# Optimization experiments

Measured on AMD Instinct MI355X. Metric: run time of the kernel, lower is better.

Reference implementation:

```python
import jax, jax.numpy as jnp
import numpy as np


def _shift(x, k):
    # roll time axis forward by k, zero-filling the first k steps
    if k == 0:
        return x
    return jnp.pad(x, ((0, 0), (k, 0), (0, 0)))[:, : x.shape[1]]


def _stu_conv(u, v, n):
    # u: (B,L,D), v: (L,K) spectral filters; non-tensordot branch of conv()
    B, L, D = u.shape
    K = v.shape[1]
    sgn = jnp.where(jnp.arange(L) % 2 == 1, -1.0, 1.0).astype(jnp.float32)[None, :, None, None]
    ue = jnp.broadcast_to(u[:, :, None, :], (B, L, K, D)).astype(jnp.float32)
    U = jnp.stack([ue, ue * sgn], axis=-1)                     # (B,L,K,D,2)
    Uf = jnp.fft.rfft(U, n=n, axis=1)
    vf = jnp.fft.rfft(v.astype(jnp.float32)[None, :, :, None, None], n=n, axis=1)
    Uc = jnp.fft.irfft(vf * Uf, n=n, axis=1)[:, :L]            # (B,L,K,D,2)
    U_plus = Uc[..., 0]
    U_minus = Uc[..., 1] * sgn
    return U_plus.astype(u.dtype), U_minus.astype(u.dtype)


def setup_inputs() -> dict:
    key = jax.random.key(0)
    ks = jax.random.split(key, 6)
    B, L, D, K, k_u, k_y = 2, 1024, 512, 16, 3, 2
    u = jax.random.normal(ks[0], (B, L, D), jnp.float32)
    filters = jax.random.normal(ks[1], (L, K), jnp.float32) / np.float32(np.sqrt(L))
    M_u = jax.random.normal(ks[2], (D, k_u, D), jnp.float32) * 0.01
    M_y = jax.random.normal(ks[3], (D, k_y, D), jnp.float32) * 0.01
    M_phi_plus = jax.random.normal(ks[4], (K, D, D), jnp.float32) * 0.01
    M_phi_minus = jax.random.normal(ks[5], (K, D, D), jnp.float32) * 0.01
    return {"u": u, "filters": filters, "M_u": M_u, "M_y": M_y,
            "M_phi_plus": M_phi_plus, "M_phi_minus": M_phi_minus}


def reference(u, filters, M_u, M_y, M_phi_plus, M_phi_minus):
    B, L, D = u.shape
    n = 1 << int(np.ceil(np.log2(2 * L - 1)))  # nearest power of two >= 2L-1
    k_u = M_u.shape[1]
    k_y = M_y.shape[1]

    # FFT-based long convolution with the +/- sign trick
    U_plus, U_minus = _stu_conv(u, filters, n)
    spectral = (jnp.einsum('blkd,kdo->blo', U_plus, M_phi_plus)
                + jnp.einsum('blkd,kdo->blo', U_minus, M_phi_minus))

    # input-AR term of compute_ar_strict: sum_j u[t+1-j] @ M_u[:, j-1].T (shifts 0..k_u-1)
    u_sh = jnp.stack([_shift(u, j - 1) for j in range(1, k_u + 1)], axis=1)  # (B,k_u,L,D)
    y_in = jnp.einsum('bjlf,ijf->bli', u_sh, M_u)

    z = spectral + y_in  # (B,L,D)

    # output-AR recurrence of compute_ar_strict as a scan
    def step(y_buf, z_t):
        y_t = z_t + jnp.einsum('bjf,djf->bd', y_buf, M_y)
        y_buf = jnp.concatenate([y_t[:, None], y_buf[:, :-1]], axis=1)
        return y_buf, y_t

    _, ys = jax.lax.scan(step, jnp.zeros((B, k_y, D), z.dtype), jnp.swapaxes(z, 0, 1))
    return jnp.swapaxes(ys, 0, 1)  # (B,L,D)
```

## Files before the change

kernel.cpp:

```cpp
#include <hip/hip_runtime.h>
#include <hip/hip_bf16.h>


using bf16 = __hip_bfloat16;
typedef __attribute__((ext_vector_type(8))) short bf16x8;
typedef __attribute__((ext_vector_type(4))) float f32x4;

#define B_   2
#define L_   1024
#define D_   512
#define K_   16
#define KT   17920
#define ROWS 2048
#define NTAP 6
#define PBLD 3584
#define SPLITD 14
#define SPLITR 6
#define ZBROWS 1032
#define NKS 40
#define NTD 20
#define WZOFF 4194304

#define WAIT_VM6 0x0F76
#define WAIT_VM4 0x0F74
#define WAIT_VM0 0x0F70

__device__ __forceinline__ void gll16(const void* g, void* l) {
    __builtin_amdgcn_global_load_lds(
        (const __attribute__((address_space(1))) unsigned int*)g,
        (__attribute__((address_space(3))) unsigned int*)l, 16, 0, 0);
}

__global__ void prep_all(const float* __restrict__ u, const float* __restrict__ fil,
                         const float* __restrict__ Mu, const float* __restrict__ My,
                         const float* __restrict__ Mp, const float* __restrict__ Mm,
                         bf16* __restrict__ U, bf16* __restrict__ BT,
                         bf16* __restrict__ PB, bf16* __restrict__ W,
                         bf16* __restrict__ Myb, bf16* __restrict__ BTT,
                         bf16* __restrict__ uPT) {
    __shared__ bf16 t[64][72];
    int bid = blockIdx.x, tid = threadIdx.x;
    auto pack4 = [](float4 v) {
        ushort4 o; bf16 h;
        h = __float2bfloat16(v.x); o.x = *(unsigned short*)&h;
        h = __float2bfloat16(v.y); o.y = *(unsigned short*)&h;
        h = __float2bfloat16(v.z); o.z = *(unsigned short*)&h;
        h = __float2bfloat16(v.w); o.w = *(unsigned short*)&h;
        return o;
    };
    if (bid < 3072) {
        int e4 = bid * 256 + tid;
        int r = e4 / 384, rem = e4 % 384;
        int tt = rem >> 7, f = (rem & 127) * 4;
        int b = r >> 10, l = r & 1023;
        float4 v = {0.f, 0.f, 0.f, 0.f};
        if (l >= tt) v = *(const float4*)&u[((size_t)b * L_ + l - tt) * D_ + f];
        *(ushort4*)&U[(size_t)r * KT + 16384 + tt * 512 + f] = pack4(v);
    } else if (bid < 3840) {
        int e4 = (bid - 3072) * 256 + tid;
        int o = e4 / 384, tf4 = (e4 % 384) * 4;
        float4 v = *(const float4*)&Mu[(size_t)o * 1536 + tf4];
        *(ushort4*)&BT[(size_t)o * KT + 16384 + tf4] = pack4(v);
    } else if (bid < 4352) {
        int e4 = (bid - 3840) * 256 + tid;
        int n = e4 >> 8, c4 = (e4 & 255) * 4;
        float4 v;
        if (c4 < 512) {
            v.x = (n == c4) ? 1.f : 0.f;     v.y = (n == c4 + 1) ? 1.f : 0.f;
            v.z = (n == c4 + 2) ? 1.f : 0.f; v.w = (n == c4 + 3) ? 1.f : 0.f;
        } else v = *(const float4*)&My[(size_t)n * 1024 + (c4 - 512)];
        *(ushort4*)&PB[(size_t)n * PBLD + c4] = pack4(v);
    } else if (bid < 5120) {
        int tile = bid - 4352;
        int set = tile >> 8, rem = tile & 255;
        int k = rem >> 4, g = (rem >> 2) & 3, kb = rem & 3;
        for (int idx = tid; idx < 4096; idx += 256) {
            int i = idx >> 5, jp = idx & 31;
            int j = ((jp >> 3) ^ ((i >> 1) & 3)) * 8 + (jp & 7);
            int x = g * 128 + i - kb * 32 - j - (set == 2 ? 1 : 0);
            float v = 0.f;
            if (x >= 0) {
                int row = (set == 0) ? 2 * x : 2 * x + 1;
                v = fil[row * K_ + k];
            }
            W[(size_t)tile * 4096 + idx] = __float2bfloat16(v);
        }
    } else if (bid < 5632) {
        int e4 = (bid - 5120) * 256 + tid;
        float4 v = *(const float4*)&My[(size_t)e4 * 4];
        *(ushort4*)&Myb[(size_t)e4 * 4] = pack4(v);
    } else if (bid < 7872) {
        int tt = bid - 5632;
        int zb = tt >> 6, rem = tt & 63;
        int bx = rem & 7, by = rem >> 3;
        int col = tid & 63, r0 = (tid >> 6) * 16;
        if (zb < 32) {
            int dt = bx * 64, ot = by * 64, c = zb;
            int k = c & 15;
            const float* sp = Mp + (size_t)k * D_ * D_;
            const float* sm = Mm + (size_t)k * D_ * D_;
            float sg = (c < 16) ? 1.f : -1.f;
            for (int i = 0; i < 16; ++i) {
                size_t o_ = (size_t)(dt + r0 + i) * D_ + ot + col;
                t[r0 + i][col] = __float2bfloat16(sp[o_] + sg * sm[o_]);
            }
            __syncthreads();
            for (int i = 0; i < 16; ++i)
                BT[(size_t)(ot + r0 + i) * KT + c * D_ + dt + col] = t[col][r0 + i];
        } else if (zb < 34) {
            int h = zb - 32;
            int dt = bx * 64, ft = by * 64;
            for (int i = 0; i < 16; ++i)
                t[r0 + i][col] = __float2bfloat16(My[(size_t)(dt + r0 + i) * 1024 + (1 - h) * 512 + ft + col]);
            __syncthreads();
            for (int i = 0; i < 16; ++i)
                BTT[(size_t)(ft + r0 + i) * 1024 + h * 512 + dt + col] = t[col][r0 + i];
        } else {
            for (int it = 0; it < 4; ++it) {
                int b = it >> 1, p = it & 1;
                int mt = bx * 64, dt = by * 64;
                __syncthreads();
                for (int i = 0; i < 16; ++i)
                    t[r0 + i][col] = __float2bfloat16(u[((size_t)b * L_ + 2 * (mt + r0 + i) + p) * D_ + dt + col]);
                __syncthreads();
                for (int i = 0; i < 16; ++i)
                    uPT[((size_t)it * 512 + dt + r0 + i) * 512 + mt + col] = t[col][r0 + i];
            }
        }
    } else {
        ushort4 z4 = {0, 0, 0, 0};
        for (int i = 0; i < 4; ++i)
            *(ushort4*)&W[(size_t)WZOFF + (size_t)(i * 256 + tid) * 4] = z4;
    }
}

__device__ __forceinline__ void phi_body(
    const bf16* A, int lda, const bf16* BT, int ldb,
    bf16* out, int ldo, int klen, const bf16* add, int lad,
    int row0, int col0, bf16* sA, bf16* sB)
{
    const int tid = threadIdx.x, lane = tid & 63, wave = tid >> 6;
    const int wm = (wave & 1) * 64, wn = (wave >> 1) * 64;
    const int ml = lane & 15, q = lane >> 4;
    const int srow = lane >> 2, scol = (((lane & 3) ^ ((srow >> 1) & 3))) * 8;
    const int swz = ((ml >> 1) & 3);
    f32x4 acc[4][4] = {};

    for (int k = 0; k < klen; k += 32) {
        __syncthreads();
        #pragma unroll
        for (int repi = 0; repi < 2; ++repi) {
            int a = wave + repi * 4;
            gll16(A  + (size_t)(row0 + a * 16 + srow) * lda + k + scol, &sA[a * 512]);
            gll16(BT + (size_t)(col0 + a * 16 + srow) * ldb + k + scol, &sB[a * 512]);
        }
        __syncthreads();
        bf16x8 af[4], bfr[4];
        #pragma unroll
        for (int i = 0; i < 4; ++i)
            af[i] = *(const bf16x8*)&sA[(wm + i * 16 + ml) * 32 + (q ^ swz) * 8];
        #pragma unroll
        for (int j = 0; j < 4; ++j)
            bfr[j] = *(const bf16x8*)&sB[(wn + j * 16 + ml) * 32 + (q ^ swz) * 8];
        #pragma unroll
        for (int i = 0; i < 4; ++i)
            #pragma unroll
            for (int j = 0; j < 4; ++j)
                acc[i][j] = __builtin_amdgcn_mfma_f32_16x16x32_bf16(af[i], bfr[j], acc[i][j], 0, 0, 0);
    }
    #pragma unroll
    for (int i = 0; i < 4; ++i)
        #pragma unroll
        for (int j = 0; j < 4; ++j)
            #pragma unroll
            for (int reg = 0; reg < 4; ++reg) {
                int r = row0 + wm + i * 16 + q * 4 + reg;
                int cc = col0 + wn + j * 16 + ml;
                float v = acc[i][j][reg];
                if (add) v += __bfloat162float(add[(size_t)r * lad + cc]);
                out[(size_t)r * ldo + cc] = __float2bfloat16(v);
            }
}

__device__ __forceinline__ void phi_body8(
    const bf16* A, int lda, const bf16* BT, int ldb,
    bf16* out, int ldo, int klen, const bf16* add, int lad,
    int row0, int col0, bf16* sA, bf16* sB)
{
    const int tid = threadIdx.x, lane = tid & 63, wave = tid >> 6;
    const int wm = (wave & 1) * 64, wn = (wave >> 1) * 64;
    const int ml = lane & 15, q = lane >> 4;
    const int srow = lane >> 2, scol = (((lane & 3) ^ ((srow >> 1) & 3))) * 8;
    const int swz = ((ml >> 1) & 3);
    f32x4 acc[4][4] = {};

    for (int k = 0; k < klen; k += 32) {
        __syncthreads();
        gll16(A  + (size_t)(row0 + wave * 16 + srow) * lda + k + scol, &sA[wave * 512]);
        gll16(BT + (size_t)(col0 + (2 * wave) * 16 + srow) * ldb + k + scol, &sB[(2 * wave) * 512]);
        gll16(BT + (size_t)(col0 + (2 * wave + 1) * 16 + srow) * ldb + k + scol, &sB[(2 * wave + 1) * 512]);
        __syncthreads();
        bf16x8 af[4], bfr[4];
        #pragma unroll
        for (int i = 0; i < 4; ++i)
            af[i] = *(const bf16x8*)&sA[(wm + i * 16 + ml) * 32 + (q ^ swz) * 8];
        #pragma unroll
        for (int j = 0; j < 4; ++j)
            bfr[j] = *(const bf16x8*)&sB[(wn + j * 16 + ml) * 32 + (q ^ swz) * 8];
        #pragma unroll
        for (int i = 0; i < 4; ++i)
            #pragma unroll
            for (int j = 0; j < 4; ++j)
                acc[i][j] = __builtin_amdgcn_mfma_f32_16x16x32_bf16(af[i], bfr[j], acc[i][j], 0, 0, 0);
    }
    #pragma unroll
    for (int i = 0; i < 4; ++i)
        #pragma unroll
        for (int j = 0; j < 4; ++j)
            #pragma unroll
            for (int reg = 0; reg < 4; ++reg) {
                int r = row0 + wm + i * 16 + q * 4 + reg;
                int cc = col0 + wn + j * 16 + ml;
                float v = acc[i][j][reg];
                if (add) v += __bfloat162float(add[(size_t)r * lad + cc]);
                out[(size_t)r * ldo + cc] = __float2bfloat16(v);
            }
}

__global__ void k_ztaps(const bf16* __restrict__ partD, float* __restrict__ z,
                        bf16* __restrict__ zbuf, bf16* PB, const bf16* BTT) {
    __shared__ bf16 sA[4096];
    __shared__ bf16 sB[4096];
    int bid = blockIdx.x;
    if (bid < 32) {
        int row0 = (bid & 3) * 128, col0 = (bid >> 2) * 128;
        phi_body(PB + 3 * 512, PBLD, BTT, 1024, PB + 5 * 512, PBLD, 1024,
                 nullptr, 0, row0, col0, sA, sB);
        return;
    }
    if (bid == 32) {
        ushort4 z4 = {0, 0, 0, 0};
        for (int i = 0; i < 8; ++i) {
            int e4 = i * 256 + threadIdx.x;
            int b = e4 >> 10, rem = e4 & 1023;
            int g = rem >> 7, c4 = (rem & 127) * 4;
            *(ushort4*)&zbuf[(size_t)(b * ZBROWS + g) * 512 + c4] = z4;
        }
        return;
    }
    int t = (bid - 33) * 256 + threadIdx.x;
    int r = t >> 7, f4 = (t & 127) * 4;
    const ushort4* p = (const ushort4*)partD;
    float4 s = {0.f, 0.f, 0.f, 0.f};
    #pragma unroll
    for (int c = 0; c < SPLITD; ++c) {
        ushort4 v = p[(size_t)c * (ROWS * D_ / 4) + t];
        s.x += __uint_as_float((unsigned)v.x << 16);
        s.y += __uint_as_float((unsigned)v.y << 16);
        s.z += __uint_as_float((unsigned)v.z << 16);
        s.w += __uint_as_float((unsigned)v.w << 16);
    }
    ((float4*)z)[t] = s;
    ushort4 zb4;
    { bf16 h;
      h = __float2bfloat16(s.x); zb4.x = *(unsigned short*)&h;
      h = __float2bfloat16(s.y); zb4.y = *(unsigned short*)&h;
      h = __float2bfloat16(s.z); zb4.z = *(unsigned short*)&h;
      h = __float2bfloat16(s.w); zb4.w = *(unsigned short*)&h; }
    int b = r >> 10, li = r & 1023;
    *(ushort4*)&zbuf[(size_t)(b * ZBROWS + 8 + li) * 512 + f4] = zb4;
}

__global__ void reduce_out(const float* __restrict__ z, const bf16* __restrict__ partR,
                           float* __restrict__ out) {
    int t = blockIdx.x * 256 + threadIdx.x;
    if (t >= ROWS * D_ / 4) return;
    float4 s = ((const float4*)z)[t];
    const ushort4* p = (const ushort4*)partR;
    #pragma unroll
    for (int c = 0; c < SPLITR; ++c) {
        ushort4 v = p[(size_t)c * (ROWS * D_ / 4) + t];
        s.x += __uint_as_float((unsigned)v.x << 16);
        s.y += __uint_as_float((unsigned)v.y << 16);
        s.z += __uint_as_float((unsigned)v.z << 16);
        s.w += __uint_as_float((unsigned)v.w << 16);
    }
    ((float4*)out)[t] = s;
}

__global__ __launch_bounds__(512, 2) void conv8(
    const bf16* __restrict__ W, const bf16* __restrict__ uPT,
    bf16* __restrict__ U,
    const bf16* PB, const bf16* BTT, const bf16* Myb)
{
    __shared__ bf16 sA[4][8192];
    __shared__ bf16 sB[4][8192];
    int id = blockIdx.x;
    const int tid = threadIdx.x, lane = tid & 63, wave = tid >> 6;
    if (id < 24) {
        int pz = id >> 3, sub = id & 7;
        int row0 = (sub & 3) * 128, col0 = (sub >> 2) * 256;
        bf16* BTTw = (bf16*)BTT; bf16* PBw = (bf16*)PB;
        if (pz == 0)
            phi_body8(PB, PBLD, BTT, 1024, PBw + 2 * 512, PBLD, 1024,
                      nullptr, 0, row0, col0, &sA[0][0], &sB[0][0]);
        else if (pz == 1)
            phi_body8(BTT + 512, 1024, Myb + 512, 1024,
                      BTTw + (size_t)512 * 1024, 1024, 512,
                      nullptr, 0, row0, col0, &sA[0][0], &sB[0][0]);
        else
            phi_body8(BTT + 512, 1024, Myb, 1024,
                      BTTw + (size_t)512 * 1024 + 512, 1024, 512,
                      BTT, 1024, row0, col0, &sA[0][0], &sB[0][0]);
        return;
    }
    const int cid = id - 24;
    const int mt2 = (cid < 256) ? 1 : 0;
    const int zc = (cid & 255) >> 1;
    const int dt2 = cid & 1;
    const int pc = zc & 3, b = (zc >> 2) & 1, k = zc >> 3;
    const int pb_ = pc & 1;
    const int p = (pc & 1) ^ (pc >> 1);
    const int set = (pc < 2) ? 0 : (pc == 2 ? 1 : 2);
    const int ch = (pc < 2) ? k : 16 + k;
    const int plane = b * 2 + pb_;
    const int nks = (mt2 + 1) * 8;
    const int NT = nks >> 1;

    const int wm = (wave >> 2) * 128;
    const int wn = (wave & 3) * 64;
    const int ml = lane & 15, q16 = lane >> 4;
    const int srow = lane >> 2, scol = (((lane & 3) ^ ((srow >> 1) & 3))) * 8;
    const int swz = ((ml >> 1) & 3);
    const int koff = (q16 ^ swz) * 8;

    const int a0 = 2 * wave, a1 = a0 + 1;
    const int rb = mt2 * 2 + (a0 >> 3);
    const bf16* wbase = W + ((size_t)(set * 16 + k) * 16) * 4096;
    const bf16* wzero = W + (size_t)WZOFF;
    const bf16* bB0 = uPT + ((size_t)plane * 512 + dt2 * 256 + a0 * 16 + srow) * 512 + scol;
    const bf16* bB1 = uPT + ((size_t)plane * 512 + dt2 * 256 + a1 * 16 + srow) * 512 + scol;

    auto stageA = [&](int s) {
        if (s >= nks) return;
        int s4 = s >> 2;
        const bf16* t0 = (rb >= s4)
            ? wbase + (size_t)((rb - s4) * 4 + (s & 3)) * 4096 : wzero;
        gll16(t0 + ((a0 & 7) * 512 + lane * 8), &sA[s & 3][a0 * 512]);
        gll16(t0 + ((a1 & 7) * 512 + lane * 8), &sA[s & 3][a1 * 512]);
    };
    auto stageB = [&](int s) {
        if (s >= nks) return;
        gll16(bB0 + s * 32, &sB[s & 3][a0 * 512]);
        gll16(bB1 + s * 32, &sB[s & 3][a1 * 512]);
    };

    f32x4 acc[8][4] = {};

    stageB(0); stageB(1); stageA(0); stageA(1);
    stageB(2); stageB(3); stageA(2);
    __builtin_amdgcn_s_waitcnt(WAIT_VM6);
    __builtin_amdgcn_s_barrier();

    for (int t = 0; t < NT; ++t) {
        const int u0 = (2 * t) & 3, u1 = u0 + 1;
        bf16x8 bfr[4][2];
        #pragma unroll
        for (int ph = 0; ph < 4; ++ph) {
            bf16x8 af[2][2];
            if (ph == 0) {
                #pragma unroll
                for (int fc = 0; fc < 4; ++fc) {
                    bfr[fc][0] = *(const bf16x8*)&sB[u0][(wn + fc * 16 + ml) * 32 + koff];
                    bfr[fc][1] = *(const bf16x8*)&sB[u1][(wn + fc * 16 + ml) * 32 + koff];
                }
            }
            #pragma unroll
            for (int f2 = 0; f2 < 2; ++f2) {
                int R = wm + (2 * ph + f2) * 16 + ml;
                af[f2][0] = *(const bf16x8*)&sA[u0][R * 32 + koff];
                af[f2][1] = *(const bf16x8*)&sA[u1][R * 32 + koff];
            }
            if (ph == 0)      stageA(2 * t + 3);
            else if (ph == 1) stageB(2 * t + 4);
            else if (ph == 2) stageB(2 * t + 5);
            else              stageA(2 * t + 4);
            __builtin_amdgcn_s_barrier();
            __builtin_amdgcn_s_setprio(1);
            #pragma unroll
            for (int f2 = 0; f2 < 2; ++f2)
                #pragma unroll
                for (int fc = 0; fc < 4; ++fc) {
                    acc[2 * ph + f2][fc] = __builtin_amdgcn_mfma_f32_16x16x32_bf16(
                        af[f2][0], bfr[fc][0], acc[2 * ph + f2][fc], 0, 0, 0);
                    acc[2 * ph + f2][fc] = __builtin_amdgcn_mfma_f32_16x16x32_bf16(
                        af[f2][1], bfr[fc][1], acc[2 * ph + f2][fc], 0, 0, 0);
                }
            __builtin_amdgcn_s_setprio(0);
            if (ph == 3) {
                if (t < NT - 2)       __builtin_amdgcn_s_waitcnt(WAIT_VM6);
                else if (t == NT - 2) __builtin_amdgcn_s_waitcnt(WAIT_VM0);
            }
            __builtin_amdgcn_s_barrier();
        }
    }

    #pragma unroll
    for (int i = 0; i < 8; ++i)
        #pragma unroll
        for (int j = 0; j < 4; ++j)
            #pragma unroll
            for (int reg = 0; reg < 4; ++reg) {
                int m = mt2 * 256 + wm + i * 16 + q16 * 4 + reg;
                int l = 2 * m + p;
                int d = dt2 * 256 + wn + j * 16 + ml;
                U[(size_t)(b * L_ + l) * KT + ch * 512 + d] = __float2bfloat16(acc[i][j][reg]);
            }
}

__global__ __launch_bounds__(512, 2) void gemm_d(
    const bf16* __restrict__ U, const bf16* __restrict__ BT,
    bf16* __restrict__ part, const bf16* PB, const bf16* BTT)
{
    __shared__ bf16 sA[4][8192];
    __shared__ bf16 sB[4][8192];
    int id = blockIdx.x;
    const int tid = threadIdx.x, lane = tid & 63, wave = tid >> 6;
    if (id < 32) {
        if (wave >= 4) {
            for (int i = 0; i < 64; ++i) __syncthreads();
            return;
        }
        int r0_ = (id & 3) * 128, c0_ = (id >> 2) * 128;
        phi_body(PB + 512, PBLD, BTT, 1024, (bf16*)PB + 3 * 512, PBLD, 1024,
                 nullptr, 0, r0_, c0_, &sA[0][0], &sB[0][0]);
        return;
    }
    id -= 32;
    const int zz = id >> 4;
    const int n_ = id & 15;
    const int row0 = (n_ >> 1) * 256, col0 = (n_ & 1) * 256;
    const int k0 = zz * (KT / SPLITD);

    const int wm = (wave >> 2) * 128;
    const int wn = (wave & 3) * 64;
    const int ml = lane & 15, q16 = lane >> 4;
    const int srow = lane >> 2, scol = (((lane & 3) ^ ((srow >> 1) & 3))) * 8;
    const int swz = ((ml >> 1) & 3);
    const int koff = (q16 ^ swz) * 8;

    const int a0 = 2 * wave, a1 = 2 * wave + 1;
    const bf16* bA0 = U  + (size_t)(row0 + a0 * 16 + srow) * KT + k0 + scol;
    const bf16* bA1 = U  + (size_t)(row0 + a1 * 16 + srow) * KT + k0 + scol;
    const bf16* bB0 = BT + (size_t)(col0 + a0 * 16 + srow) * KT + k0 + scol;
    const bf16* bB1 = BT + (size_t)(col0 + a1 * 16 + srow) * KT + k0 + scol;
    auto stageA = [&](int s) {
        if (s >= NKS) return;
        gll16(bA0 + s * 32, &sA[s & 3][a0 * 512]);
        gll16(bA1 + s * 32, &sA[s & 3][a1 * 512]);
    };
    auto stageB = [&](int s) {
        if (s >= NKS) return;
        gll16(bB0 + s * 32, &sB[s & 3][a0 * 512]);
        gll16(bB1 + s * 32, &sB[s & 3][a1 * 512]);
    };

    f32x4 acc[8][4] = {};

    stageB(0); stageB(1); stageA(0); stageA(1);
    stageB(2); stageB(3); stageA(2);
    __builtin_amdgcn_s_waitcnt(WAIT_VM6);
    __builtin_amdgcn_s_barrier();

    for (int t = 0; t < NTD; ++t) {
        const int u0 = (2 * t) & 3, u1 = u0 + 1;
        bf16x8 bfr[4][2];
        #pragma unroll
        for (int ph = 0; ph < 4; ++ph) {
            bf16x8 af[2][2];
            if (ph == 0) {
                #pragma unroll
                for (int fc = 0; fc < 4; ++fc) {
                    bfr[fc][0] = *(const bf16x8*)&sB[u0][(wn + fc * 16 + ml) * 32 + koff];
                    bfr[fc][1] = *(const bf16x8*)&sB[u1][(wn + fc * 16 + ml) * 32 + koff];
                }
            }
            #pragma unroll
            for (int f2 = 0; f2 < 2; ++f2) {
                int R = wm + (2 * ph + f2) * 16 + ml;
                af[f2][0] = *(const bf16x8*)&sA[u0][R * 32 + koff];
                af[f2][1] = *(const bf16x8*)&sA[u1][R * 32 + koff];
            }
            if (ph == 0)      stageA(2 * t + 3);
            else if (ph == 1) stageB(2 * t + 4);
            else if (ph == 2) stageB(2 * t + 5);
            else              stageA(2 * t + 4);
            __builtin_amdgcn_s_barrier();
            __builtin_amdgcn_s_setprio(1);
            #pragma unroll
            for (int f2 = 0; f2 < 2; ++f2)
                #pragma unroll
                for (int fc = 0; fc < 4; ++fc) {
                    acc[2 * ph + f2][fc] = __builtin_amdgcn_mfma_f32_16x16x32_bf16(
                        af[f2][0], bfr[fc][0], acc[2 * ph + f2][fc], 0, 0, 0);
                    acc[2 * ph + f2][fc] = __builtin_amdgcn_mfma_f32_16x16x32_bf16(
                        af[f2][1], bfr[fc][1], acc[2 * ph + f2][fc], 0, 0, 0);
                }
            __builtin_amdgcn_s_setprio(0);
            if (ph == 3) {
                if (t < NTD - 2)       __builtin_amdgcn_s_waitcnt(WAIT_VM6);
                else if (t == NTD - 2) __builtin_amdgcn_s_waitcnt(WAIT_VM0);
            }
            __builtin_amdgcn_s_barrier();
        }
    }

    bf16* o = part + (size_t)zz * ROWS * D_;
    #pragma unroll
    for (int i = 0; i < 8; ++i)
        #pragma unroll
        for (int j = 0; j < 4; ++j)
            #pragma unroll
            for (int reg = 0; reg < 4; ++reg) {
                int r = row0 + wm + i * 16 + q16 * 4 + reg;
                int cc = col0 + wn + j * 16 + ml;
                o[(size_t)r * D_ + cc] = __float2bfloat16(acc[i][j][reg]);
            }
}

__device__ __forceinline__ void mm128_pair(
    const bf16* Abase, int alda, const bf16* Bbase, int ldb, int n,
    bf16* o, int row0, int col0, bf16 (*sA)[4096], bf16 (*sB)[4096])
{
    const int tid = threadIdx.x, lane = tid & 63, wave = tid >> 6;
    const int wm = (wave & 1) * 64, wn = (wave >> 1) * 64;
    const int ml = lane & 15, q = lane >> 4;
    const int srow = lane >> 2, scol = (((lane & 3) ^ ((srow >> 1) & 3))) * 8;
    const int swz = ((ml >> 1) & 3);
    f32x4 acc[4][4] = {};

    const bf16* bA0 = Abase + (size_t)(wave * 16 + srow) * alda + scol;
    const bf16* bA1 = Abase + (size_t)((wave + 4) * 16 + srow) * alda + scol;
    const bf16* bB0 = Bbase + (size_t)(wave * 16 + srow) * ldb + scol;
    const bf16* bB1 = Bbase + (size_t)((wave + 4) * 16 + srow) * ldb + scol;
    auto stage = [&](int s) {
        int buf = s & 3;
        gll16(bA0 + s * 32, &sA[buf][wave * 512]);
        gll16(bA1 + s * 32, &sA[buf][(wave + 4) * 512]);
        gll16(bB0 + s * 32, &sB[buf][wave * 512]);
        gll16(bB1 + s * 32, &sB[buf][(wave + 4) * 512]);
    };
    auto compute = [&](int c) {
        bf16x8 af[4], bfr[4];
        #pragma unroll
        for (int i = 0; i < 4; ++i)
            af[i] = *(const bf16x8*)&sA[c][(wm + i * 16 + ml) * 32 + (q ^ swz) * 8];
        #pragma unroll
        for (int j = 0; j < 4; ++j)
            bfr[j] = *(const bf16x8*)&sB[c][(wn + j * 16 + ml) * 32 + (q ^ swz) * 8];
        #pragma unroll
        for (int i = 0; i < 4; ++i)
            #pragma unroll
            for (int j = 0; j < 4; ++j)
                acc[i][j] = __builtin_amdgcn_mfma_f32_16x16x32_bf16(af[i], bfr[j], acc[i][j], 0, 0, 0);
    };
    stage(0); stage(1);
    const int npair = n >> 1;
    for (int p = 0; p < npair; ++p) {
        __builtin_amdgcn_s_waitcnt(WAIT_VM0);
        __builtin_amdgcn_s_barrier();
        if (2 * p + 2 < n) { stage(2 * p + 2); stage(2 * p + 3); }
        compute((2 * p) & 3);
        compute((2 * p + 1) & 3);
    }
    #pragma unroll
    for (int i = 0; i < 4; ++i)
        #pragma unroll
        for (int j = 0; j < 4; ++j)
            #pragma unroll
            for (int reg = 0; reg < 4; ++reg) {
                int r = row0 + wm + i * 16 + q * 4 + reg;
                int cc = col0 + wn + j * 16 + ml;
                o[(size_t)r * D_ + cc] = __float2bfloat16(acc[i][j][reg]);
            }
}

__global__ __launch_bounds__(256, 2) void gemm_r(
    const bf16* __restrict__ zbuf, const bf16* __restrict__ BT,
    bf16* __restrict__ part)
{
    __shared__ bf16 sA[4][4096];
    __shared__ bf16 sB[4][4096];
    const int row0 = blockIdx.x * 128, col0 = blockIdx.y * 128;
    const int zz = blockIdx.z;
    const int s = 1 + zz;
    const int b = row0 >> 10, li0 = row0 & 1023;
    mm128_pair(zbuf + ((size_t)(b * ZBROWS + 8 + li0 - s)) * 512, 512,
               BT + (size_t)col0 * PBLD + (size_t)zz * 512, PBLD,
               16, part + (size_t)zz * ROWS * D_, row0, col0, sA, sB);
}

extern "C" void kernel_launch(void* const* d_in, const int* in_sizes, int n_in,
                              void* d_out, int out_size, void* d_ws, size_t ws_size,
                              hipStream_t stream) {
    const float* u   = (const float*)d_in[0];
    const float* fil = (const float*)d_in[1];
    const float* Mu  = (const float*)d_in[2];
    const float* My  = (const float*)d_in[3];
    const float* Mp  = (const float*)d_in[4];
    const float* Mm  = (const float*)d_in[5];
    float* out = (float*)d_out;

    char* ws = (char*)d_ws;
    size_t off = 0;
    auto alloc = [&](size_t bytes) { void* p = ws + off; off = (off + bytes + 255) & ~(size_t)255; return p; };
    bf16*  U    = (bf16*) alloc((size_t)ROWS * KT * 2);
    bf16*  BT   = (bf16*) alloc((size_t)512 * KT * 2);
    bf16*  PB   = (bf16*) alloc((size_t)512 * PBLD * 2);
    bf16*  BTT  = (bf16*) alloc((size_t)1024 * 1024 * 2);
    bf16*  Myb  = (bf16*) alloc((size_t)512 * 1024 * 2);
    float* z    = (float*)alloc((size_t)ROWS * D_ * 4);
    bf16*  zb   = (bf16*) alloc((size_t)B_ * ZBROWS * 512 * 2);
    char*  region = (char*)alloc((size_t)16 * ROWS * D_ * 2);
    bf16*  W    = (bf16*)region;
    bf16*  uPT  = (bf16*)(region + (size_t)768 * 4096 * 2);
    bf16*  partD = (bf16*)region;
    bf16*  partR = (bf16*)region;

    prep_all<<<7873, 256, 0, stream>>>(u, fil, Mu, My, Mp, Mm,
                                       U, BT, PB, W, Myb, BTT, uPT);

    conv8<<<536, 512, 0, stream>>>(W, uPT, U, PB, BTT, Myb);

    gemm_d<<<256, 512, 0, stream>>>(U, BT, partD, PB, BTT);

    k_ztaps<<<1057, 256, 0, stream>>>(partD, z, zb, PB, BTT);

    gemm_r<<<dim3(16, 4, SPLITR), 256, 0, stream>>>(zb, PB + 512, partR);

    reduce_out<<<(ROWS * D_ / 4 + 255) / 256, 256, 0, stream>>>(z, partR, out);
}
```

Before: 231.7 us.

## Double-buffer A fragments in MFMA loops and fold phi blocks into conv blocks

The conv8 and gemm_d inner loops now read the next A fragment set from LDS into a second register buffer while the current set feeds the MFMAs, so LDS reads overlap with matrix math instead of serialising each phase. Separately, the 24 phi_body8 tiles no longer get their own blocks. They run as a prologue inside 24 of the light (mt2=0) conv blocks, which cuts the grid from 536 to 512 blocks. This trades extra register pressure and a longer tail on those 24 blocks for better latency hiding and fewer launched blocks.

```diff
diff --git a/kernel.cpp b/kernel.cpp
--- a/kernel.cpp
+++ b/kernel.cpp
@@ -22,7 +22,6 @@
 #define WZOFF 4194304
 
 #define WAIT_VM6 0x0F76
-#define WAIT_VM4 0x0F74
 #define WAIT_VM0 0x0F70
 
 __device__ __forceinline__ void gll16(const void* g, void* l) {
@@ -297,9 +296,10 @@
     __shared__ bf16 sB[4][8192];
     int id = blockIdx.x;
     const int tid = threadIdx.x, lane = tid & 63, wave = tid >> 6;
-    if (id < 24) {
-        int pz = id >> 3, sub = id & 7;
-        int row0 = (sub & 3) * 128, col0 = (sub >> 2) * 256;
+    if (id >= 256 && id < 280) {
+        int sub = id - 256;
+        int pz = sub >> 3, s8 = sub & 7;
+        int row0 = (s8 & 3) * 128, col0 = (s8 >> 2) * 256;
         bf16* BTTw = (bf16*)BTT; bf16* PBw = (bf16*)PB;
         if (pz == 0)
             phi_body8(PB, PBLD, BTT, 1024, PBw + 2 * 512, PBLD, 1024,
@@ -312,11 +312,11 @@
             phi_body8(BTT + 512, 1024, Myb, 1024,
                       BTTw + (size_t)512 * 1024 + 512, 1024, 512,
                       BTT, 1024, row0, col0, &sA[0][0], &sB[0][0]);
-        return;
-    }
-    const int cid = id - 24;
-    const int mt2 = (cid < 256) ? 1 : 0;
-    const int zc = (cid & 255) >> 1;
+        __syncthreads();
+    }
+    const int cid = (id < 256) ? id : id - 256;
+    const int mt2 = (id < 256) ? 1 : 0;
+    const int zc = cid >> 1;
     const int dt2 = cid & 1;
     const int pc = zc & 3, b = (zc >> 2) & 1, k = zc >> 3;
     const int pb_ = pc & 1;
@@ -356,6 +356,36 @@
     };
 
     f32x4 acc[8][4] = {};
+    bf16x8 bfr[4][2], afA[2][2], afB[2][2];
+
+    auto readB = [&](int u0, int u1) {
+        #pragma unroll
+        for (int fc = 0; fc < 4; ++fc) {
+            bfr[fc][0] = *(const bf16x8*)&sB[u0][(wn + fc * 16 + ml) * 32 + koff];
+            bfr[fc][1] = *(const bf16x8*)&sB[u1][(wn + fc * 16 + ml) * 32 + koff];
+        }
+    };
+    auto readA = [&](bf16x8 (&af)[2][2], int u0, int u1, int q) {
+        #pragma unroll
+        for (int f2 = 0; f2 < 2; ++f2) {
+            int R = wm + (2 * q + f2) * 16 + ml;
+            af[f2][0] = *(const bf16x8*)&sA[u0][R * 32 + koff];
+            af[f2][1] = *(const bf16x8*)&sA[u1][R * 32 + koff];
+        }
+    };
+    auto mfma8 = [&](bf16x8 (&af)[2][2], int q) {
+        __builtin_amdgcn_s_setprio(1);
+        #pragma unroll
+        for (int f2 = 0; f2 < 2; ++f2)
+            #pragma unroll
+            for (int fc = 0; fc < 4; ++fc) {
+                acc[2 * q + f2][fc] = __builtin_amdgcn_mfma_f32_16x16x32_bf16(
+                    af[f2][0], bfr[fc][0], acc[2 * q + f2][fc], 0, 0, 0);
+                acc[2 * q + f2][fc] = __builtin_amdgcn_mfma_f32_16x16x32_bf16(
+                    af[f2][1], bfr[fc][1], acc[2 * q + f2][fc], 0, 0, 0);
+            }
+        __builtin_amdgcn_s_setprio(0);
+    };
 
     stageB(0); stageB(1); stageA(0); stageA(1);
     stageB(2); stageB(3); stageA(2);
@@ -364,45 +394,29 @@
 
     for (int t = 0; t < NT; ++t) {
         const int u0 = (2 * t) & 3, u1 = u0 + 1;
-        bf16x8 bfr[4][2];
-        #pragma unroll
-        for (int ph = 0; ph < 4; ++ph) {
-            bf16x8 af[2][2];
-            if (ph == 0) {
-                #pragma unroll
-                for (int fc = 0; fc < 4; ++fc) {
-                    bfr[fc][0] = *(const bf16x8*)&sB[u0][(wn + fc * 16 + ml) * 32 + koff];
-                    bfr[fc][1] = *(const bf16x8*)&sB[u1][(wn + fc * 16 + ml) * 32 + koff];
-                }
-            }
-            #pragma unroll
-            for (int f2 = 0; f2 < 2; ++f2) {
-                int R = wm + (2 * ph + f2) * 16 + ml;
-                af[f2][0] = *(const bf16x8*)&sA[u0][R * 32 + koff];
-                af[f2][1] = *(const bf16x8*)&sA[u1][R * 32 + koff];
-            }
-            if (ph == 0)      stageA(2 * t + 3);
-            else if (ph == 1) stageB(2 * t + 4);
-            else if (ph == 2) stageB(2 * t + 5);
-            else              stageA(2 * t + 4);
-            __builtin_amdgcn_s_barrier();
-            __builtin_amdgcn_s_setprio(1);
-            #pragma unroll
-            for (int f2 = 0; f2 < 2; ++f2)
-                #pragma unroll
-                for (int fc = 0; fc < 4; ++fc) {
-                    acc[2 * ph + f2][fc] = __builtin_amdgcn_mfma_f32_16x16x32_bf16(
-                        af[f2][0], bfr[fc][0], acc[2 * ph + f2][fc], 0, 0, 0);
-                    acc[2 * ph + f2][fc] = __builtin_amdgcn_mfma_f32_16x16x32_bf16(
-                        af[f2][1], bfr[fc][1], acc[2 * ph + f2][fc], 0, 0, 0);
-                }
-            __builtin_amdgcn_s_setprio(0);
-            if (ph == 3) {
-                if (t < NT - 2)       __builtin_amdgcn_s_waitcnt(WAIT_VM6);
-                else if (t == NT - 2) __builtin_amdgcn_s_waitcnt(WAIT_VM0);
-            }
-            __builtin_amdgcn_s_barrier();
-        }
+        readB(u0, u1);
+        readA(afA, u0, u1, 0);
+        readA(afB, u0, u1, 1);
+        stageA(2 * t + 3);
+        __builtin_amdgcn_s_barrier();
+        mfma8(afA, 0);
+        __builtin_amdgcn_s_barrier();
+        readA(afA, u0, u1, 2);
+        stageB(2 * t + 4);
+        __builtin_amdgcn_s_barrier();
+        mfma8(afB, 1);
+        __builtin_amdgcn_s_barrier();
+        readA(afB, u0, u1, 3);
+        stageB(2 * t + 5);
+        __builtin_amdgcn_s_barrier();
+        mfma8(afA, 2);
+        __builtin_amdgcn_s_barrier();
+        stageA(2 * t + 4);
+        __builtin_amdgcn_s_barrier();
+        mfma8(afB, 3);
+        if (t < NT - 2)       __builtin_amdgcn_s_waitcnt(WAIT_VM6);
+        else if (t == NT - 2) __builtin_amdgcn_s_waitcnt(WAIT_VM0);
+        __builtin_amdgcn_s_barrier();
     }
 
     #pragma unroll
@@ -466,6 +480,36 @@
     };
 
     f32x4 acc[8][4] = {};
+    bf16x8 bfr[4][2], afA[2][2], afB[2][2];
+
+    auto readB = [&](int u0, int u1) {
+        #pragma unroll
+        for (int fc = 0; fc < 4; ++fc) {
+            bfr[fc][0] = *(const bf16x8*)&sB[u0][(wn + fc * 16 + ml) * 32 + koff];
+            bfr[fc][1] = *(const bf16x8*)&sB[u1][(wn + fc * 16 + ml) * 32 + koff];
+        }
+    };
+    auto readA = [&](bf16x8 (&af)[2][2], int u0, int u1, int q) {
+        #pragma unroll
+        for (int f2 = 0; f2 < 2; ++f2) {
+            int R = wm + (2 * q + f2) * 16 + ml;
+            af[f2][0] = *(const bf16x8*)&sA[u0][R * 32 + koff];
+            af[f2][1] = *(const bf16x8*)&sA[u1][R * 32 + koff];
+        }
+    };
+    auto mfma8 = [&](bf16x8 (&af)[2][2], int q) {
+        __builtin_amdgcn_s_setprio(1);
+        #pragma unroll
+        for (int f2 = 0; f2 < 2; ++f2)
+            #pragma unroll
+            for (int fc = 0; fc < 4; ++fc) {
+                acc[2 * q + f2][fc] = __builtin_amdgcn_mfma_f32_16x16x32_bf16(
+                    af[f2][0], bfr[fc][0], acc[2 * q + f2][fc], 0, 0, 0);
+                acc[2 * q + f2][fc] = __builtin_amdgcn_mfma_f32_16x16x32_bf16(
+                    af[f2][1], bfr[fc][1], acc[2 * q + f2][fc], 0, 0, 0);
+            }
+        __builtin_amdgcn_s_setprio(0);
+    };
 
     stageB(0); stageB(1); stageA(0); stageA(1);
     stageB(2); stageB(3); stageA(2);
@@ -474,45 +518,29 @@
 
     for (int t = 0; t < NTD; ++t) {
         const int u0 = (2 * t) & 3, u1 = u0 + 1;
-        bf16x8 bfr[4][2];
-        #pragma unroll
-        for (int ph = 0; ph < 4; ++ph) {
-            bf16x8 af[2][2];
-            if (ph == 0) {
-                #pragma unroll
-                for (int fc = 0; fc < 4; ++fc) {
-                    bfr[fc][0] = *(const bf16x8*)&sB[u0][(wn + fc * 16 + ml) * 32 + koff];
-                    bfr[fc][1] = *(const bf16x8*)&sB[u1][(wn + fc * 16 + ml) * 32 + koff];
-                }
-            }
-            #pragma unroll
-            for (int f2 = 0; f2 < 2; ++f2) {
-                int R = wm + (2 * ph + f2) * 16 + ml;
-                af[f2][0] = *(const bf16x8*)&sA[u0][R * 32 + koff];
-                af[f2][1] = *(const bf16x8*)&sA[u1][R * 32 + koff];
-            }
-            if (ph == 0)      stageA(2 * t + 3);
-            else if (ph == 1) stageB(2 * t + 4);
-            else if (ph == 2) stageB(2 * t + 5);
-            else              stageA(2 * t + 4);
-            __builtin_amdgcn_s_barrier();
-            __builtin_amdgcn_s_setprio(1);
-            #pragma unroll
-            for (int f2 = 0; f2 < 2; ++f2)
-                #pragma unroll
-                for (int fc = 0; fc < 4; ++fc) {
-                    acc[2 * ph + f2][fc] = __builtin_amdgcn_mfma_f32_16x16x32_bf16(
-                        af[f2][0], bfr[fc][0], acc[2 * ph + f2][fc], 0, 0, 0);
-                    acc[2 * ph + f2][fc] = __builtin_amdgcn_mfma_f32_16x16x32_bf16(
-                        af[f2][1], bfr[fc][1], acc[2 * ph + f2][fc], 0, 0, 0);
-                }
-            __builtin_amdgcn_s_setprio(0);
-            if (ph == 3) {
-                if (t < NTD - 2)       __builtin_amdgcn_s_waitcnt(WAIT_VM6);
-                else if (t == NTD - 2) __builtin_amdgcn_s_waitcnt(WAIT_VM0);
-            }
-            __builtin_amdgcn_s_barrier();
-        }
+        readB(u0, u1);
+        readA(afA, u0, u1, 0);
+        readA(afB, u0, u1, 1);
+        stageA(2 * t + 3);
+        __builtin_amdgcn_s_barrier();
+        mfma8(afA, 0);
+        __builtin_amdgcn_s_barrier();
+        readA(afA, u0, u1, 2);
+        stageB(2 * t + 4);
+        __builtin_amdgcn_s_barrier();
+        mfma8(afB, 1);
+        __builtin_amdgcn_s_barrier();
+        readA(afB, u0, u1, 3);
+        stageB(2 * t + 5);
+        __builtin_amdgcn_s_barrier();
+        mfma8(afA, 2);
+        __builtin_amdgcn_s_barrier();
+        stageA(2 * t + 4);
+        __builtin_amdgcn_s_barrier();
+        mfma8(afB, 3);
+        if (t < NTD - 2)       __builtin_amdgcn_s_waitcnt(WAIT_VM6);
+        else if (t == NTD - 2) __builtin_amdgcn_s_waitcnt(WAIT_VM0);
+        __builtin_amdgcn_s_barrier();
     }
 
     bf16* o = part + (size_t)zz * ROWS * D_;
@@ -630,7 +658,7 @@
     prep_all<<<7873, 256, 0, stream>>>(u, fil, Mu, My, Mp, Mm,
                                        U, BT, PB, W, Myb, BTT, uPT);
 
-    conv8<<<536, 512, 0, stream>>>(W, uPT, U, PB, BTT, Myb);
+    conv8<<<512, 512, 0, stream>>>(W, uPT, U, PB, BTT, Myb);
 
     gemm_d<<<256, 512, 0, stream>>>(U, BT, partD, PB, BTT);
 
```

New measurement: 252.1 us. +8.8%, slower.
